# Optimization experiments

Measured on AMD Instinct MI355X. Metric: run time of the kernel, lower is better.

Reference implementation:

```python
import jax, jax.numpy as jnp
import numpy as np

GAMMA = 0.99
EPS = 1e-05
B, D, K, C = 65536, 512, 1024, 100


def setup_inputs() -> dict:
    key = jax.random.key(0)
    k1, k2, k3, k4, k5 = jax.random.split(key, 5)
    return {
        "batch_vectors": jax.random.normal(k1, (B, D), dtype=jnp.float32),
        "batch_keys_id": jax.random.randint(k2, (B,), 0, C, dtype=jnp.int32),
        "weight": jax.random.normal(k3, (D, K), dtype=jnp.float32),
        "cluster_size": jnp.ones((K,), dtype=jnp.float32),
        "embed_avg": jax.random.normal(k4, (D, K), dtype=jnp.float32),
        "hist": jax.random.uniform(k5, (K, C), dtype=jnp.float32),
    }


def reference(batch_vectors, batch_keys_id, weight, cluster_size, embed_avg, hist):
    # --- find_nearest_centroids: euclidean distance to each codebook column ---
    x_sq = jnp.sum(batch_vectors * batch_vectors, axis=1, keepdims=True)      # [B,1]
    w_sq = jnp.sum(weight * weight, axis=0, keepdims=True)                    # [1,K]
    d2 = x_sq - 2.0 * (batch_vectors @ weight) + w_sq                         # [B,K]
    dist = jnp.sqrt(jnp.maximum(d2, 0.0))
    argmin = jnp.argmin(dist, axis=-1)                                        # [B]

    # --- one-hot counts and embed_sum (scatter-add form of flatten @ onehot) ---
    n_idx_choice = jax.ops.segment_sum(
        jnp.ones((B,), dtype=batch_vectors.dtype), argmin, num_segments=K)    # [K]
    n_idx_choice = jnp.where(n_idx_choice == 0, 1.0, n_idx_choice)
    embed_sum = jax.ops.segment_sum(batch_vectors, argmin, num_segments=K).T  # [D,K]

    # --- EMA updates ---
    new_cluster_size = cluster_size * GAMMA + (1.0 - GAMMA) * n_idx_choice
    new_embed_avg = embed_avg * GAMMA + (1.0 - GAMMA) * embed_sum
    n = jnp.sum(new_cluster_size)
    cs_norm = (new_cluster_size + EPS) / (n + K * EPS) * n                    # [K]
    new_weight = new_embed_avg / cs_norm[None, :]                             # [D,K]

    # --- update_hist: per-cluster class histogram (scatter-add) ---
    batch_hist = jnp.zeros((K, C), dtype=hist.dtype).at[argmin, batch_keys_id].add(1.0)
    new_hist = hist * GAMMA + (1.0 - GAMMA) * batch_hist

    return new_weight, new_cluster_size, new_embed_avg, new_hist, argmin
```

## Files before the change

kernel.cpp:

```cpp
#include <hip/hip_runtime.h>
#include <hip/hip_fp16.h>


#define NB 65536
#define ND 512
#define NK 1024
#define NC 100
#define TAU 0.25f
#define FLAG_CAP 16384
#define FROWS 8
#define GROWS 128

typedef unsigned int u32;
typedef unsigned short u16;
typedef unsigned long long u64;
typedef __attribute__((ext_vector_type(8))) _Float16 half8v;
typedef __attribute__((ext_vector_type(4))) float f32x4;

#define OFF_COUNTS   0
#define OFF_CURSOR   1024
#define OFF_BHIST    2048
#define OFF_FLAGCNT  104448
#define OFF_WSQ      104512
#define OFF_ZERO_END 105536
#define OFF_FLAGLIST 105536
#define OFF_FKEYS    121920
#define OFF_CSNORM   154688
#define OFF_OFFSETS  155712
#define OFF_ARGMIN   156736
#define OFF_ORDER    222272
#define OFF_KORDER   287808
#define OFF_WTHI     353344
#define OFF_WT32     615488
#define OFF_XH       1139776
#define OFF_ESUM     17916992

__device__ inline f32x4 mfma16f(half8v a, half8v b, f32x4 c) {
  return __builtin_amdgcn_mfma_f32_16x16x32_f16(a, b, c, 0, 0, 0);
}

__device__ __forceinline__ void gl_lds16(const u16* g, u16* l) {
  __builtin_amdgcn_global_load_lds(
      (const __attribute__((address_space(1))) u32*)g,
      (__attribute__((address_space(3))) u32*)l, 16, 0, 0);
}

__device__ inline u32 f32_sortable(float f) {
  u32 b = __float_as_uint(f);
  return (b & 0x80000000u) ? ~b : (b | 0x80000000u);
}

__device__ inline half8v cvt8_f16(const float4& a, const float4& b) {
  half8v h;
  h[0] = (_Float16)a.x; h[1] = (_Float16)a.y;
  h[2] = (_Float16)a.z; h[3] = (_Float16)a.w;
  h[4] = (_Float16)b.x; h[5] = (_Float16)b.y;
  h[6] = (_Float16)b.z; h[7] = (_Float16)b.w;
  return h;
}

__global__ __launch_bounds__(256) void prep_all(const float* __restrict__ W,
                                                const float* __restrict__ X,
                                                u16* __restrict__ Wthi,
                                                float* __restrict__ Wt32,
                                                u16* __restrict__ Xh,
                                                float* __restrict__ wsq) {
  __shared__ float tile[32][33];
  int t = threadIdx.x;
  if (blockIdx.x >= 512) {
    size_t i = ((size_t)(blockIdx.x - 512) * 256 + t) * 8;
    float4 a = *(const float4*)(X + i);
    float4 b = *(const float4*)(X + i + 4);
    *(half8v*)(Xh + i) = cvt8_f16(a, b);
    return;
  }
  int db = blockIdx.x & 15;
  int kb = blockIdx.x >> 4;
  int tx = t & 31, ty = t >> 5;
  float s = 0.f;
#pragma unroll
  for (int i = 0; i < 4; ++i) {
    int d = db * 32 + ty + 8 * i;
    float wv = W[(size_t)d * NK + kb * 32 + tx];
    tile[ty + 8 * i][tx] = wv;
    s += wv * wv;
  }
  atomicAdd(&wsq[kb * 32 + tx], s);
  __syncthreads();
#pragma unroll
  for (int i = 0; i < 4; ++i) {
    int kl = ty + 8 * i;
    float f = tile[tx][kl];
    size_t o = (size_t)(kb * 32 + kl) * ND + db * 32 + tx;
    Wt32[o] = f;
    Wthi[o] = __half_as_ushort(__float2half(f));
  }
}

__global__ __launch_bounds__(256, 2) void argmin_pair(
    const u16* __restrict__ Xh, const u16* __restrict__ Wthi,
    const float* __restrict__ wsq, const int* __restrict__ cls,
    int* __restrict__ argmin_i, float* __restrict__ argmin_f,
    int* __restrict__ counts, float* __restrict__ bhist,
    int* __restrict__ flagCnt, int* __restrict__ flagList) {
  __shared__ __align__(16) u16 Ah[2 * 128 * 64];
  __shared__ __align__(16) u16 Bh[2 * 128 * 64];
  __shared__ float wsq_s[NK];
  __shared__ float redV[128][2];
  __shared__ float redS[128][2];
  __shared__ int redI[128][2];

  const int t = threadIdx.x;
  const int lane = t & 63;
  const int w = t >> 6;
  const int g = lane >> 4;
  const int l15 = lane & 15;
  const int wrb = (w >> 1) * 64;
  const int wcb = (w & 1) * 128;
  const int brow = blockIdx.x * 128;

#pragma unroll
  for (int i = 0; i < 4; ++i) wsq_s[t + 256 * i] = wsq[t + 256 * i];

  const int sub = lane >> 3;
  const int c8p = lane & 7;
  const size_t asrc = (size_t)(brow + w * 32 + sub) * ND + (size_t)((c8p ^ sub) * 8);

  const size_t bsrc = (size_t)(2 * (w * 32 + sub) + (c8p >> 2)) * ND +
                      (size_t)(((c8p & 3) ^ (sub & 3)) * 8);

  int aofs[2];
#pragma unroll
  for (int kk = 0; kk < 2; ++kk)
    aofs[kk] = (wrb + l15) * 64 + (((kk * 4 + g) ^ (l15 & 7)) * 8);
  const int bofs = wcb * 32 + (l15 >> 1) * 64 + (l15 & 1) * 32 +
                   ((g ^ ((l15 >> 1) & 3)) * 8);

  float bestV[4][4], secV[4][4];
  int bestI[4][4];
#pragma unroll
  for (int m = 0; m < 4; ++m)
#pragma unroll
    for (int r = 0; r < 4; ++r) {
      bestV[m][r] = 3.4e38f; secV[m][r] = 3.4e38f; bestI[m][r] = 0;
    }

  f32x4 acc[4][8];
#pragma unroll
  for (int m = 0; m < 4; ++m)
#pragma unroll
    for (int n = 0; n < 8; ++n) acc[m][n] = (f32x4)0.f;

#define ISSUE_A(kc_, ab_)                                                \
  {                                                                      \
    const u16* as_ = Xh + asrc + (kc_) * 64;                             \
    u16* ad_ = Ah + (ab_) * 8192 + w * 32 * 64;                          \
    _Pragma("unroll")                                                    \
    for (int q = 0; q < 4; ++q)                                          \
      gl_lds16(as_ + (size_t)(q * 8) * ND, ad_ + q * 8 * 64);            \
  }
#define ISSUE_B(ct_, sk_, bb_)                                           \
  {                                                                      \
    const u16* bs_ = Wthi + (size_t)(ct_) * 256 * ND + bsrc + (sk_) * 32;\
    u16* bd_ = Bh + (bb_) * 8192 + w * 32 * 64;                          \
    _Pragma("unroll")                                                    \
    for (int q = 0; q < 4; ++q)                                          \
      gl_lds16(bs_ + (size_t)(q * 16) * ND, bd_ + q * 8 * 64);           \
  }
#define DRAIN asm volatile("s_waitcnt vmcnt(0) lgkmcnt(0)" ::: "memory")

  ISSUE_A(0, 0);
  ISSUE_B(0, 0, 0);
  DRAIN;
  __syncthreads();

  for (int s = 0; s < 64; ++s) {
    const int sk = s & 15;
    const int kpar = s & 1;
    const int abuf = (s >> 1) & 1;
    const int bbuf = s & 1;
    if (s < 63) {
      const int s1 = s + 1;
      ISSUE_B(s1 >> 4, s1 & 15, s1 & 1);
      if (s & 1) ISSUE_A(((s1 & 15) >> 1), (s1 >> 1) & 1);
    }
    const u16* Ab = Ah + abuf * 8192;
    const u16* Bb = Bh + bbuf * 8192;
    {
      half8v a_h[4];
#pragma unroll
      for (int m = 0; m < 4; ++m)
        a_h[m] = *(const half8v*)&Ab[aofs[kpar] + m * 1024];
#pragma unroll
      for (int n = 0; n < 8; ++n) {
        half8v b_h = *(const half8v*)&Bb[bofs + n * 512];
#pragma unroll
        for (int m = 0; m < 4; ++m)
          acc[m][n] = mfma16f(a_h[m], b_h, acc[m][n]);
      }
    }
    if (sk == 15) {
      const int ct = s >> 4;
#pragma unroll
      for (int n = 0; n < 8; ++n) {
        int col = ct * 256 + wcb + 16 * n + l15;
        float wq = wsq_s[col];
#pragma unroll
        for (int m = 0; m < 4; ++m)
#pragma unroll
          for (int r = 0; r < 4; ++r) {
            float v = wq - 2.0f * acc[m][n][r];
            if (v < bestV[m][r]) {
              secV[m][r] = bestV[m][r];
              bestV[m][r] = v;
              bestI[m][r] = col;
            } else if (v < secV[m][r]) {
              secV[m][r] = v;
            }
          }
      }
#pragma unroll
      for (int m = 0; m < 4; ++m)
#pragma unroll
        for (int n = 0; n < 8; ++n) acc[m][n] = (f32x4)0.f;
    }
    DRAIN;
    __syncthreads();
  }
#undef ISSUE_A
#undef ISSUE_B
#undef DRAIN

#pragma unroll
  for (int m = 0; m < 4; ++m)
#pragma unroll
    for (int r = 0; r < 4; ++r) {
      float v = bestV[m][r];
      float sec = secV[m][r];
      int idx = bestI[m][r];
#pragma unroll
      for (int mask = 1; mask < 16; mask <<= 1) {
        float ov = __shfl_xor(v, mask, 64);
        float os = __shfl_xor(sec, mask, 64);
        int oi = __shfl_xor(idx, mask, 64);
        float nsec = fminf(fminf(sec, os), fmaxf(v, ov));
        if (ov < v || (ov == v && oi < idx)) { v = ov; idx = oi; }
        sec = nsec;
      }
      if (l15 == 0) {
        int rowl = wrb + 16 * m + 4 * g + r;
        redV[rowl][w & 1] = v;
        redS[rowl][w & 1] = sec;
        redI[rowl][w & 1] = idx;
      }
    }
  __syncthreads();
  if (t < 128) {
    float v0 = redV[t][0], v1 = redV[t][1];
    float s0 = redS[t][0], s1 = redS[t][1];
    int i0 = redI[t][0], i1 = redI[t][1];
    float bv, sec;
    int bi;
    if (v1 < v0 || (v1 == v0 && i1 < i0)) { bv = v1; bi = i1; }
    else { bv = v0; bi = i0; }
    sec = fminf(fminf(s0, s1), fmaxf(v0, v1));
    int b = brow + t;
    argmin_i[b] = bi;
    argmin_f[b] = (float)bi;
    atomicAdd(&counts[bi], 1);
    atomicAdd(&bhist[(size_t)bi * NC + cls[b]], 1.0f);
    if (sec - bv < TAU) {
      int slot = atomicAdd(flagCnt, 1);
      if (slot < FLAG_CAP) flagList[slot] = b;
    }
  }
}

__global__ __launch_bounds__(256) void fixup_kernel(
    const float* __restrict__ X, const float* __restrict__ Wt32,
    const float* __restrict__ wsq, const int* __restrict__ flagCnt,
    const int* __restrict__ flagList, const int* __restrict__ cls,
    int* __restrict__ argmin_i, float* __restrict__ argmin_f,
    int* __restrict__ counts, float* __restrict__ bhist) {
  __shared__ float xs[FROWS][ND];
  __shared__ int rows[FROWS];
  __shared__ u64 wred[4][FROWS];
  int n = *flagCnt;
  if (n > FLAG_CAP) n = FLAG_CAP;
  int r0 = blockIdx.x * FROWS;
  if (r0 >= n) return;
  int nr = n - r0; if (nr > FROWS) nr = FROWS;
  int t = threadIdx.x;
  if (t < FROWS) rows[t] = flagList[r0 + (t < nr ? t : 0)];
  __syncthreads();
  for (int j = t; j < FROWS * (ND / 4); j += 256) {
    int r = j >> 7, c = j & 127;
    ((float4*)xs[r])[c] = ((const float4*)(X + (size_t)rows[r] * ND))[c];
  }
  __syncthreads();

  const int k0 = t * 4;
  const float4* w0 = (const float4*)(Wt32 + (size_t)(k0 + 0) * ND);
  const float4* w1 = (const float4*)(Wt32 + (size_t)(k0 + 1) * ND);
  const float4* w2 = (const float4*)(Wt32 + (size_t)(k0 + 2) * ND);
  const float4* w3 = (const float4*)(Wt32 + (size_t)(k0 + 3) * ND);
  float a[4][FROWS];
#pragma unroll
  for (int kk = 0; kk < 4; ++kk)
#pragma unroll
    for (int r = 0; r < FROWS; ++r) a[kk][r] = 0.f;

  for (int d = 0; d < ND / 4; ++d) {
    float4 v0 = w0[d], v1 = w1[d], v2 = w2[d], v3 = w3[d];
#pragma unroll
    for (int r = 0; r < FROWS; ++r) {
      float4 x4 = ((const float4*)xs[r])[d];
      a[0][r] += x4.x * v0.x + x4.y * v0.y + x4.z * v0.z + x4.w * v0.w;
      a[1][r] += x4.x * v1.x + x4.y * v1.y + x4.z * v1.z + x4.w * v1.w;
      a[2][r] += x4.x * v2.x + x4.y * v2.y + x4.z * v2.z + x4.w * v2.w;
      a[3][r] += x4.x * v3.x + x4.y * v3.y + x4.z * v3.z + x4.w * v3.w;
    }
  }

  float wq0 = wsq[k0], wq1 = wsq[k0 + 1], wq2 = wsq[k0 + 2], wq3 = wsq[k0 + 3];
  const int wv_ = t >> 6, lane = t & 63;
#pragma unroll
  for (int r = 0; r < FROWS; ++r) {
    float bv = wq0 - 2.0f * a[0][r];
    int bk = k0;
    float v;
    v = wq1 - 2.0f * a[1][r]; if (v < bv) { bv = v; bk = k0 + 1; }
    v = wq2 - 2.0f * a[2][r]; if (v < bv) { bv = v; bk = k0 + 2; }
    v = wq3 - 2.0f * a[3][r]; if (v < bv) { bv = v; bk = k0 + 3; }
    u64 key = ((u64)f32_sortable(bv) << 32) | (u32)bk;
#pragma unroll
    for (int m = 1; m < 64; m <<= 1) {
      u64 o = __shfl_xor(key, m, 64);
      if (o < key) key = o;
    }
    if (lane == 0) wred[wv_][r] = key;
  }
  __syncthreads();
  if (t < nr) {
    u64 k = wred[0][t];
    if (wred[1][t] < k) k = wred[1][t];
    if (wred[2][t] < k) k = wred[2][t];
    if (wred[3][t] < k) k = wred[3][t];
    int nk = (int)(u32)(k & 0xffffffffu);
    int row = rows[t];
    int old = argmin_i[row];
    if (nk != old) {
      argmin_i[row] = nk;
      argmin_f[row] = (float)nk;
      atomicSub(&counts[old], 1);
      atomicAdd(&counts[nk], 1);
      int c = cls[row];
      atomicAdd(&bhist[(size_t)old * NC + c], -1.0f);
      atomicAdd(&bhist[(size_t)nk * NC + c], 1.0f);
    }
  }
}

__global__ __launch_bounds__(1024) void scan_kernel(
    const int* __restrict__ counts, const float* __restrict__ cluster_size,
    float* __restrict__ out_ncs, float* __restrict__ csnorm,
    int* __restrict__ offsets) {
  __shared__ float wsum[16];
  __shared__ int wcnt[16];
  int t = threadIdx.x, lane = t & 63, wv = t >> 6;
  int cnt = counts[t];
  float ncs = cluster_size[t] * 0.99f + 0.01f * (cnt == 0 ? 1.0f : (float)cnt);
  out_ncs[t] = ncs;

  float s = ncs;
#pragma unroll
  for (int m = 1; m < 64; m <<= 1) s += __shfl_xor(s, m, 64);
  int ic = cnt;
#pragma unroll
  for (int o = 1; o < 64; o <<= 1) {
    int v = __shfl_up(ic, o, 64);
    if (lane >= o) ic += v;
  }
  if (lane == 63) { wsum[wv] = s; wcnt[wv] = ic; }
  __syncthreads();
  float n = 0.f;
  int coff = 0;
  for (int i = 0; i < 16; ++i) {
    n += wsum[i];
    if (i < wv) coff += wcnt[i];
  }
  csnorm[t] = (ncs + 1e-5f) / (n + 1024.0f * 1e-5f) * n;
  offsets[t] = coff + ic - cnt;
}

__global__ __launch_bounds__(256) void reorder_kernel(
    const int* __restrict__ argmin_i, const int* __restrict__ offsets,
    int* __restrict__ cursor, int* __restrict__ order,
    int* __restrict__ korder, float* __restrict__ esum) {
  int b = blockIdx.x * 256 + threadIdx.x;
  float4 z = make_float4(0.f, 0.f, 0.f, 0.f);
  *(float4*)(esum + (size_t)b * 8) = z;
  *(float4*)(esum + (size_t)b * 8 + 4) = z;
  int k = argmin_i[b];
  int pos = atomicAdd(&cursor[k], 1);
  int o = offsets[k] + pos;
  order[o] = b;
  korder[o] = k;
}

__global__ __launch_bounds__(256) void gather_runs(
    const float* __restrict__ X, const int* __restrict__ order,
    const int* __restrict__ korder, float* __restrict__ esum) {
  __shared__ int so[GROWS];
  __shared__ int sk[GROWS];
  int t = threadIdx.x;
  int base = blockIdx.x * GROWS;
  if (t < GROWS) {
    so[t] = order[base + t];
    sk[t] = korder[base + t];
  }
  __syncthreads();
  float a0 = 0.f, a1 = 0.f;
  int curk = sk[0];
#pragma unroll 8
  for (int m = 0; m < GROWS; ++m) {
    int k = sk[m];
    if (k != curk) {
      atomicAdd(&esum[(size_t)curk * ND + 2 * t], a0);
      atomicAdd(&esum[(size_t)curk * ND + 2 * t + 1], a1);
      a0 = 0.f; a1 = 0.f; curk = k;
    }
    float2 v = *(const float2*)(X + (size_t)so[m] * ND + 2 * t);
    a0 += v.x;
    a1 += v.y;
  }
  atomicAdd(&esum[(size_t)curk * ND + 2 * t], a0);
  atomicAdd(&esum[(size_t)curk * ND + 2 * t + 1], a1);
}

__global__ __launch_bounds__(256) void ema_hist_kernel(
    const float* __restrict__ esum, const float* __restrict__ embed_avg,
    const float* __restrict__ csnorm, const float* __restrict__ hist,
    const float* __restrict__ bhist, float* __restrict__ out_w,
    float* __restrict__ out_ea, float* __restrict__ out_hist) {
  __shared__ float tile[32][33];
  int t = threadIdx.x;
  if (blockIdx.x >= 512) {
    int i = (blockIdx.x - 512) * 256 + t;
    out_hist[i] = hist[i] * 0.99f + 0.01f * bhist[i];
    return;
  }
  int kb = blockIdx.x & 31;
  int db = blockIdx.x >> 5;
  int tx = t & 31, ty = t >> 5;
#pragma unroll
  for (int i = 0; i < 4; ++i) {
    int kl = ty + i * 8;
    tile[kl][tx] = esum[(size_t)(kb * 32 + kl) * ND + db * 32 + tx];
  }
  __syncthreads();
#pragma unroll
  for (int i = 0; i < 4; ++i) {
    int d = db * 32 + ty + i * 8;
    int k = kb * 32 + tx;
    size_t idx = (size_t)d * NK + k;
    float nea = embed_avg[idx] * 0.99f + 0.01f * tile[tx][ty + i * 8];
    out_ea[idx] = nea;
    out_w[idx] = nea / csnorm[k];
  }
}

extern "C" void kernel_launch(void* const* d_in, const int* in_sizes, int n_in,
                              void* d_out, int out_size, void* d_ws, size_t ws_size,
                              hipStream_t stream) {
  const float* X = (const float*)d_in[0];
  const int* cls = (const int*)d_in[1];
  const float* W = (const float*)d_in[2];
  const float* cluster_size = (const float*)d_in[3];
  const float* embed_avg = (const float*)d_in[4];
  const float* hist = (const float*)d_in[5];

  float* wsf = (float*)d_ws;
  int* wsi = (int*)d_ws;
  int* counts = wsi + OFF_COUNTS;
  int* cursor = wsi + OFF_CURSOR;
  float* bhist = wsf + OFF_BHIST;
  int* flagCnt = wsi + OFF_FLAGCNT;
  float* wsq = wsf + OFF_WSQ;
  int* flagList = wsi + OFF_FLAGLIST;
  float* csnorm = wsf + OFF_CSNORM;
  int* offsets = wsi + OFF_OFFSETS;
  int* argmin_i = wsi + OFF_ARGMIN;
  int* order = wsi + OFF_ORDER;
  int* korder = wsi + OFF_KORDER;
  u16* Wthi = (u16*)(wsf + OFF_WTHI);
  float* Wt32 = wsf + OFF_WT32;
  u16* Xh = (u16*)(wsf + OFF_XH);
  float* esum = wsf + OFF_ESUM;

  float* out = (float*)d_out;
  float* out_w = out;
  float* out_ncs = out + (size_t)ND * NK;
  float* out_ea = out_ncs + NK;
  float* out_hist = out_ea + (size_t)ND * NK;
  float* out_arg = out_hist + (size_t)NK * NC;

  hipMemsetAsync(d_ws, 0, (size_t)OFF_ZERO_END * 4, stream);

  prep_all<<<512 + NB * ND / 8 / 256, 256, 0, stream>>>(W, X, Wthi, Wt32, Xh,
                                                        wsq);
  argmin_pair<<<NB / 128, 256, 0, stream>>>(Xh, Wthi, wsq, cls, argmin_i,
                                            out_arg, counts, bhist, flagCnt,
                                            flagList);
  fixup_kernel<<<FLAG_CAP / FROWS, 256, 0, stream>>>(X, Wt32, wsq, flagCnt,
                                                     flagList, cls, argmin_i,
                                                     out_arg, counts, bhist);
  scan_kernel<<<1, 1024, 0, stream>>>(counts, cluster_size, out_ncs, csnorm,
                                      offsets);
  reorder_kernel<<<NB / 256, 256, 0, stream>>>(argmin_i, offsets, cursor, order,
                                               korder, esum);
  gather_runs<<<NB / GROWS, 256, 0, stream>>>(X, order, korder, esum);
  ema_hist_kernel<<<512 + (NK * NC) / 256, 256, 0, stream>>>(
      esum, embed_avg, csnorm, hist, bhist, out_w, out_ea, out_hist);
}
```

Measured before the change: 360.9 us.

## Deepen argmin GEMM pipeline to triple-buffered B with partial vmcnt waits

Moves the B-tile (codebook) staging from double to triple buffering, prefetching two k-steps ahead, and replaces the full vmcnt(0)/lgkmcnt(0) drain each iteration with partial vmcnt waits and a bare s_barrier. The goal is to keep global-to-LDS loads in flight across iterations and hide memory latency in the main distance GEMM. To fit LDS, the wsq shared copy is dropped (read from global instead) and the reduction scratch arrays alias the B buffer after the loop. Risks include read/write races from the weaker barrier and extra global loads for wsq.

```diff
diff --git a/kernel.cpp b/kernel.cpp
--- a/kernel.cpp
+++ b/kernel.cpp
@@ -24,7 +24,6 @@
 #define OFF_WSQ      104512
 #define OFF_ZERO_END 105536
 #define OFF_FLAGLIST 105536
-#define OFF_FKEYS    121920
 #define OFF_CSNORM   154688
 #define OFF_OFFSETS  155712
 #define OFF_ARGMIN   156736
@@ -97,18 +96,14 @@
   }
 }
 
-__global__ __launch_bounds__(256, 2) void argmin_pair(
+__global__ __launch_bounds__(256, 2) void argmin_deep(
     const u16* __restrict__ Xh, const u16* __restrict__ Wthi,
     const float* __restrict__ wsq, const int* __restrict__ cls,
     int* __restrict__ argmin_i, float* __restrict__ argmin_f,
     int* __restrict__ counts, float* __restrict__ bhist,
     int* __restrict__ flagCnt, int* __restrict__ flagList) {
   __shared__ __align__(16) u16 Ah[2 * 128 * 64];
-  __shared__ __align__(16) u16 Bh[2 * 128 * 64];
-  __shared__ float wsq_s[NK];
-  __shared__ float redV[128][2];
-  __shared__ float redS[128][2];
-  __shared__ int redI[128][2];
+  __shared__ __align__(16) u16 Bh[3 * 128 * 64];
 
   const int t = threadIdx.x;
   const int lane = t & 63;
@@ -119,9 +114,6 @@
   const int wcb = (w & 1) * 128;
   const int brow = blockIdx.x * 128;
 
-#pragma unroll
-  for (int i = 0; i < 4; ++i) wsq_s[t + 256 * i] = wsq[t + 256 * i];
-
   const int sub = lane >> 3;
   const int c8p = lane & 7;
   const size_t asrc = (size_t)(brow + w * 32 + sub) * ND + (size_t)((c8p ^ sub) * 8);
@@ -151,9 +143,9 @@
 #pragma unroll
     for (int n = 0; n < 8; ++n) acc[m][n] = (f32x4)0.f;
 
-#define ISSUE_A(kc_, ab_)                                                \
+#define ISSUE_A(ch_, ab_)                                                \
   {                                                                      \
-    const u16* as_ = Xh + asrc + (kc_) * 64;                             \
+    const u16* as_ = Xh + asrc + (ch_) * 64;                             \
     u16* ad_ = Ah + (ab_) * 8192 + w * 32 * 64;                          \
     _Pragma("unroll")                                                    \
     for (int q = 0; q < 4; ++q)                                          \
@@ -167,22 +159,30 @@
     for (int q = 0; q < 4; ++q)                                          \
       gl_lds16(bs_ + (size_t)(q * 16) * ND, bd_ + q * 8 * 64);           \
   }
-#define DRAIN asm volatile("s_waitcnt vmcnt(0) lgkmcnt(0)" ::: "memory")
+#define FENCE_BAR                                                        \
+  __builtin_amdgcn_sched_barrier(0);                                     \
+  __builtin_amdgcn_s_barrier();                                          \
+  __builtin_amdgcn_sched_barrier(0)
 
   ISSUE_A(0, 0);
   ISSUE_B(0, 0, 0);
-  DRAIN;
-  __syncthreads();
-
+  ISSUE_B(0, 1, 1);
+  asm volatile("s_waitcnt vmcnt(4) lgkmcnt(0)" ::: "memory");
+  FENCE_BAR;
+
+  int bbuf = 0;
   for (int s = 0; s < 64; ++s) {
     const int sk = s & 15;
     const int kpar = s & 1;
     const int abuf = (s >> 1) & 1;
-    const int bbuf = s & 1;
-    if (s < 63) {
-      const int s1 = s + 1;
-      ISSUE_B(s1 >> 4, s1 & 15, s1 & 1);
-      if (s & 1) ISSUE_A(((s1 & 15) >> 1), (s1 >> 1) & 1);
+    if (s + 2 < 64) {
+      const int s2 = s + 2;
+      int nb = bbuf + 2; if (nb >= 3) nb -= 3;
+      ISSUE_B(s2 >> 4, s2 & 15, nb);
+    }
+    if (!(s & 1) && s <= 60) {
+      const int j1 = (s >> 1) + 1;
+      ISSUE_A(j1 & 7, j1 & 1);
     }
     const u16* Ab = Ah + abuf * 8192;
     const u16* Bb = Bh + bbuf * 8192;
@@ -204,7 +204,7 @@
 #pragma unroll
       for (int n = 0; n < 8; ++n) {
         int col = ct * 256 + wcb + 16 * n + l15;
-        float wq = wsq_s[col];
+        float wq = wsq[col];
 #pragma unroll
         for (int m = 0; m < 4; ++m)
 #pragma unroll
@@ -224,12 +224,22 @@
 #pragma unroll
         for (int n = 0; n < 8; ++n) acc[m][n] = (f32x4)0.f;
     }
-    DRAIN;
-    __syncthreads();
+    if (!(s & 1) && s <= 60)
+      asm volatile("s_waitcnt vmcnt(8)" ::: "memory");
+    else if (s < 62)
+      asm volatile("s_waitcnt vmcnt(4)" ::: "memory");
+    else
+      asm volatile("s_waitcnt vmcnt(0)" ::: "memory");
+    FENCE_BAR;
+    bbuf = (bbuf + 1 == 3) ? 0 : bbuf + 1;
   }
 #undef ISSUE_A
 #undef ISSUE_B
-#undef DRAIN
+#undef FENCE_BAR
+
+  float (*redV)[2] = (float (*)[2])(Bh);
+  float (*redS)[2] = (float (*)[2])(Bh + 512);
+  int (*redI)[2] = (int (*)[2])(Bh + 1024);
 
 #pragma unroll
   for (int m = 0; m < 4; ++m)
@@ -509,7 +519,7 @@
 
   prep_all<<<512 + NB * ND / 8 / 256, 256, 0, stream>>>(W, X, Wthi, Wt32, Xh,
                                                         wsq);
-  argmin_pair<<<NB / 128, 256, 0, stream>>>(Xh, Wthi, wsq, cls, argmin_i,
+  argmin_deep<<<NB / 128, 256, 0, stream>>>(Xh, Wthi, wsq, cls, argmin_i,
                                             out_arg, counts, bhist, flagCnt,
                                             flagList);
   fixup_kernel<<<FLAG_CAP / FROWS, 256, 0, stream>>>(X, Wt32, wsq, flagCnt,
```

After: 363.5 us. Within noise of the previous version (+0.7%).

## Fold scan into reorder and EMA kernels; gather embed sums from fp16 X

Applied to the files above, without the earlier changes.

Removes the single-block scan kernel. Each reorder block now recomputes the exclusive prefix of cluster counts in shared memory, and each EMA block recomputes the cluster-size total and its csnorm slice. gather_runs now reads the fp16 copy of X already produced for the distance GEMM, halving gather memory traffic. The trade-offs are redundant per-block scans and reduced precision in embed_sum accumulation inputs.

```diff
diff --git a/kernel.cpp b/kernel.cpp
--- a/kernel.cpp
+++ b/kernel.cpp
@@ -24,12 +24,6 @@
 #define OFF_WSQ      104512
 #define OFF_ZERO_END 105536
 #define OFF_FLAGLIST 105536
-#define OFF_FKEYS    121920
-#define OFF_CSNORM   154688
-#define OFF_OFFSETS  155712
-#define OFF_ARGMIN   156736
-#define OFF_ORDER    222272
-#define OFF_KORDER   287808
 #define OFF_WTHI     353344
 #define OFF_WT32     615488
 #define OFF_XH       1139776
@@ -125,7 +119,6 @@
   const int sub = lane >> 3;
   const int c8p = lane & 7;
   const size_t asrc = (size_t)(brow + w * 32 + sub) * ND + (size_t)((c8p ^ sub) * 8);
-
   const size_t bsrc = (size_t)(2 * (w * 32 + sub) + (c8p >> 2)) * ND +
                       (size_t)(((c8p & 3) ^ (sub & 3)) * 8);
 
@@ -361,55 +354,48 @@
   }
 }
 
-__global__ __launch_bounds__(1024) void scan_kernel(
-    const int* __restrict__ counts, const float* __restrict__ cluster_size,
-    float* __restrict__ out_ncs, float* __restrict__ csnorm,
-    int* __restrict__ offsets) {
-  __shared__ float wsum[16];
-  __shared__ int wcnt[16];
+__global__ __launch_bounds__(256) void reorder_kernel(
+    const int* __restrict__ argmin_i, const int* __restrict__ counts,
+    int* __restrict__ cursor, int* __restrict__ order,
+    int* __restrict__ korder, float* __restrict__ esum) {
+  __shared__ int offs[NK];
+  __shared__ int wpart[4];
   int t = threadIdx.x, lane = t & 63, wv = t >> 6;
-  int cnt = counts[t];
-  float ncs = cluster_size[t] * 0.99f + 0.01f * (cnt == 0 ? 1.0f : (float)cnt);
-  out_ncs[t] = ncs;
-
-  float s = ncs;
-#pragma unroll
-  for (int m = 1; m < 64; m <<= 1) s += __shfl_xor(s, m, 64);
-  int ic = cnt;
+  int b = blockIdx.x * 256 + t;
+
+  float4 z = make_float4(0.f, 0.f, 0.f, 0.f);
+  *(float4*)(esum + (size_t)b * 8) = z;
+  *(float4*)(esum + (size_t)b * 8 + 4) = z;
+
+  int4 c4 = ((const int4*)counts)[t];
+  int lsum = c4.x + c4.y + c4.z + c4.w;
+  int ic = lsum;
 #pragma unroll
   for (int o = 1; o < 64; o <<= 1) {
     int v = __shfl_up(ic, o, 64);
     if (lane >= o) ic += v;
   }
-  if (lane == 63) { wsum[wv] = s; wcnt[wv] = ic; }
-  __syncthreads();
-  float n = 0.f;
-  int coff = 0;
-  for (int i = 0; i < 16; ++i) {
-    n += wsum[i];
-    if (i < wv) coff += wcnt[i];
-  }
-  csnorm[t] = (ncs + 1e-5f) / (n + 1024.0f * 1e-5f) * n;
-  offsets[t] = coff + ic - cnt;
-}
-
-__global__ __launch_bounds__(256) void reorder_kernel(
-    const int* __restrict__ argmin_i, const int* __restrict__ offsets,
-    int* __restrict__ cursor, int* __restrict__ order,
-    int* __restrict__ korder, float* __restrict__ esum) {
-  int b = blockIdx.x * 256 + threadIdx.x;
-  float4 z = make_float4(0.f, 0.f, 0.f, 0.f);
-  *(float4*)(esum + (size_t)b * 8) = z;
-  *(float4*)(esum + (size_t)b * 8 + 4) = z;
+  if (lane == 63) wpart[wv] = ic;
+  __syncthreads();
+  int woff = 0;
+  for (int i = 0; i < 4; ++i)
+    if (i < wv) woff += wpart[i];
+  int excl = woff + ic - lsum;
+  offs[t * 4 + 0] = excl;
+  offs[t * 4 + 1] = excl + c4.x;
+  offs[t * 4 + 2] = excl + c4.x + c4.y;
+  offs[t * 4 + 3] = excl + c4.x + c4.y + c4.z;
+  __syncthreads();
+
   int k = argmin_i[b];
   int pos = atomicAdd(&cursor[k], 1);
-  int o = offsets[k] + pos;
+  int o = offs[k] + pos;
   order[o] = b;
   korder[o] = k;
 }
 
 __global__ __launch_bounds__(256) void gather_runs(
-    const float* __restrict__ X, const int* __restrict__ order,
+    const u16* __restrict__ Xh, const int* __restrict__ order,
     const int* __restrict__ korder, float* __restrict__ esum) {
   __shared__ int so[GROWS];
   __shared__ int sk[GROWS];
@@ -430,9 +416,9 @@
       atomicAdd(&esum[(size_t)curk * ND + 2 * t + 1], a1);
       a0 = 0.f; a1 = 0.f; curk = k;
     }
-    float2 v = *(const float2*)(X + (size_t)so[m] * ND + 2 * t);
-    a0 += v.x;
-    a1 += v.y;
+    u32 pr = *(const u32*)(Xh + (size_t)so[m] * ND + 2 * t);
+    a0 += __half2float(__ushort_as_half((u16)(pr & 0xffffu)));
+    a1 += __half2float(__ushort_as_half((u16)(pr >> 16)));
   }
   atomicAdd(&esum[(size_t)curk * ND + 2 * t], a0);
   atomicAdd(&esum[(size_t)curk * ND + 2 * t + 1], a1);
@@ -440,10 +426,13 @@
 
 __global__ __launch_bounds__(256) void ema_hist_kernel(
     const float* __restrict__ esum, const float* __restrict__ embed_avg,
-    const float* __restrict__ csnorm, const float* __restrict__ hist,
-    const float* __restrict__ bhist, float* __restrict__ out_w,
-    float* __restrict__ out_ea, float* __restrict__ out_hist) {
+    const int* __restrict__ counts, const float* __restrict__ cluster_size,
+    const float* __restrict__ hist, const float* __restrict__ bhist,
+    float* __restrict__ out_w, float* __restrict__ out_ea,
+    float* __restrict__ out_ncs, float* __restrict__ out_hist) {
   __shared__ float tile[32][33];
+  __shared__ float csn_s[32];
+  __shared__ float wpart[4];
   int t = threadIdx.x;
   if (blockIdx.x >= 512) {
     int i = (blockIdx.x - 512) * 256 + t;
@@ -453,10 +442,37 @@
   int kb = blockIdx.x & 31;
   int db = blockIdx.x >> 5;
   int tx = t & 31, ty = t >> 5;
+  int lane = t & 63, wv = t >> 6;
+
+  int4 c4 = ((const int4*)counts)[t];
+  float4 cs4 = ((const float4*)cluster_size)[t];
+  float n0 = cs4.x * 0.99f + 0.01f * (c4.x == 0 ? 1.0f : (float)c4.x);
+  float n1 = cs4.y * 0.99f + 0.01f * (c4.y == 0 ? 1.0f : (float)c4.y);
+  float n2 = cs4.z * 0.99f + 0.01f * (c4.z == 0 ? 1.0f : (float)c4.z);
+  float n3 = cs4.w * 0.99f + 0.01f * (c4.w == 0 ? 1.0f : (float)c4.w);
+  float ps = ((n0 + n1) + (n2 + n3));
+#pragma unroll
+  for (int m = 1; m < 64; m <<= 1) ps += __shfl_xor(ps, m, 64);
+  if (lane == 0) wpart[wv] = ps;
+
 #pragma unroll
   for (int i = 0; i < 4; ++i) {
     int kl = ty + i * 8;
     tile[kl][tx] = esum[(size_t)(kb * 32 + kl) * ND + db * 32 + tx];
+  }
+  __syncthreads();
+  float n = wpart[0] + wpart[1] + wpart[2] + wpart[3];
+  if (db == 0) {
+    out_ncs[t * 4 + 0] = n0;
+    out_ncs[t * 4 + 1] = n1;
+    out_ncs[t * 4 + 2] = n2;
+    out_ncs[t * 4 + 3] = n3;
+  }
+  if (t < 32) {
+    int k = kb * 32 + t;
+    int cnt = counts[k];
+    float ncs = cluster_size[k] * 0.99f + 0.01f * (cnt == 0 ? 1.0f : (float)cnt);
+    csn_s[t] = (ncs + 1e-5f) / (n + 1024.0f * 1e-5f) * n;
   }
   __syncthreads();
 #pragma unroll
@@ -466,7 +482,7 @@
     size_t idx = (size_t)d * NK + k;
     float nea = embed_avg[idx] * 0.99f + 0.01f * tile[tx][ty + i * 8];
     out_ea[idx] = nea;
-    out_w[idx] = nea / csnorm[k];
+    out_w[idx] = nea / csn_s[tx];
   }
 }
 
@@ -488,15 +504,13 @@
   int* flagCnt = wsi + OFF_FLAGCNT;
   float* wsq = wsf + OFF_WSQ;
   int* flagList = wsi + OFF_FLAGLIST;
-  float* csnorm = wsf + OFF_CSNORM;
-  int* offsets = wsi + OFF_OFFSETS;
-  int* argmin_i = wsi + OFF_ARGMIN;
-  int* order = wsi + OFF_ORDER;
-  int* korder = wsi + OFF_KORDER;
+  int* order = wsi + 222272;
+  int* korder = wsi + 287808;
   u16* Wthi = (u16*)(wsf + OFF_WTHI);
   float* Wt32 = wsf + OFF_WT32;
   u16* Xh = (u16*)(wsf + OFF_XH);
   float* esum = wsf + OFF_ESUM;
+  int* argmin_i = wsi + 156736;
 
   float* out = (float*)d_out;
   float* out_w = out;
@@ -515,11 +529,10 @@
   fixup_kernel<<<FLAG_CAP / FROWS, 256, 0, stream>>>(X, Wt32, wsq, flagCnt,
                                                      flagList, cls, argmin_i,
                                                      out_arg, counts, bhist);
-  scan_kernel<<<1, 1024, 0, stream>>>(counts, cluster_size, out_ncs, csnorm,
-                                      offsets);
-  reorder_kernel<<<NB / 256, 256, 0, stream>>>(argmin_i, offsets, cursor, order,
+  reorder_kernel<<<NB / 256, 256, 0, stream>>>(argmin_i, counts, cursor, order,
                                                korder, esum);
-  gather_runs<<<NB / GROWS, 256, 0, stream>>>(X, order, korder, esum);
+  gather_runs<<<NB / GROWS, 256, 0, stream>>>(Xh, order, korder, esum);
   ema_hist_kernel<<<512 + (NK * NC) / 256, 256, 0, stream>>>(
-      esum, embed_avg, csnorm, hist, bhist, out_w, out_ea, out_hist);
-}
+      esum, embed_avg, counts, cluster_size, hist, bhist, out_w, out_ea,
+      out_ncs, out_hist);
+}
```

Measured after the change: 360.9 us. No clear change (+0.0%).
